# Performance work log

Measured on AMD Instinct MI355X. Metric: run time of the kernel, lower is better.

Reference implementation:

```python
import jax, jax.numpy as jnp
import numpy as np

D_OUT = 256  # out_channels; fourier dim F = D_OUT (Wr has F/2 rows)

def _fourier_pos(H, W, Wr, w1, b1, w2, b2):
    # normalized (H,W) grid in [-1,1], shape [L,2]
    ys = jnp.linspace(-1.0, 1.0, H)
    xs = jnp.linspace(-1.0, 1.0, W)
    gy, gx = jnp.meshgrid(ys, xs, indexing='ij')
    grid = jnp.stack([gy, gx], axis=-1).reshape(-1, 2)  # [L,2]
    proj = grid @ Wr.T                                   # [L,F/2]
    F = 2 * Wr.shape[0]
    feats = jnp.concatenate([jnp.cos(proj), jnp.sin(proj)], axis=-1) / jnp.sqrt(jnp.float32(F))
    h = jax.nn.gelu(feats @ w1.T + b1)
    return h @ w2.T + b2                                 # [L,D_OUT]

def setup_inputs() -> dict:
    key = jax.random.key(0)
    ks = jax.random.split(key, 11)
    N, D, H, W = 16, 256, 128, 128
    s = 1.0 / np.sqrt(D)
    return {
        'x': jax.random.normal(ks[0], (N, D, H, W), jnp.float32),
        'query': jax.random.normal(ks[1], (D_OUT,), jnp.float32),
        'k_w': jax.random.normal(ks[2], (D_OUT, D), jnp.float32) * s,
        'k_b': jax.random.normal(ks[3], (D_OUT,), jnp.float32) * 0.01,
        'v_w': jax.random.normal(ks[4], (D_OUT, D), jnp.float32) * s,
        'v_b': jax.random.normal(ks[5], (D_OUT,), jnp.float32) * 0.01,
        'Wr': jax.random.normal(ks[6], (D_OUT // 2, 2), jnp.float32),
        'w1': jax.random.normal(ks[7], (D_OUT, D_OUT), jnp.float32) * (1.0 / np.sqrt(D_OUT)),
        'b1': jax.random.normal(ks[8], (D_OUT,), jnp.float32) * 0.01,
        'w2': jax.random.normal(ks[9], (D_OUT, D_OUT), jnp.float32) * (1.0 / np.sqrt(D_OUT)),
        'b2': jax.random.normal(ks[10], (D_OUT,), jnp.float32) * 0.01,
    }

def reference(x, query, k_w, k_b, v_w, v_b, Wr, w1, b1, w2, b2):
    N, D, H, W = x.shape
    L = H * W
    tok = x.reshape(N, D, L).transpose(0, 2, 1)          # [N,L,D]
    pos = _fourier_pos(H, W, Wr, w1, b1, w2, b2)         # [L,D_OUT]
    K = tok @ k_w.T + k_b + pos[None]                    # [N,L,D_OUT]
    V = tok @ v_w.T + v_b                                # [N,L,D_OUT]
    scores = jnp.einsum('nld,d->nl', K, query) / jnp.sqrt(jnp.float32(query.shape[0]))
    attn = jax.nn.softmax(scores, axis=1)                # [N,L]
    return jnp.einsum('nl,nld->nd', attn, V)             # [N,D_OUT]
```

## Files before the change

kernel.cpp:

```cpp
#include <hip/hip_runtime.h>
#include <math.h>

#define NB 16
#define DD 256
#define LL 16384
#define DO 256

#define WS_QK    0
#define WS_QW2   256
#define WS_C1    512
#define WS_C2    513
#define WS_W1T   768
#define WS_VWT   (WS_W1T + 65536)
#define WS_PQ    (WS_VWT + 65536)
#define WS_M     (WS_PQ + LL)
#define WS_DEN   (WS_M + NB*32)
#define WS_NUM   (WS_DEN + NB*32)

__device__ __forceinline__ float gelu_tanh(float u) {
    float u3 = u*u*u;
    return 0.5f*u*(1.0f + tanhf(0.7978845608028654f*(u + 0.044715f*u3)));
}

__global__ __launch_bounds__(256) void k0a(const float* __restrict__ query,
        const float* __restrict__ k_w, const float* __restrict__ k_b,
        const float* __restrict__ w2, const float* __restrict__ b2,
        float* __restrict__ ws) {
    __shared__ float q_s[DO];
    __shared__ float red[256];
    int t = threadIdx.x;
    q_s[t] = query[t];
    __syncthreads();
    float aqk = 0.f, aqw = 0.f;
    for (int o = 0; o < DO; ++o) {
        aqk += k_w[o*DD + t] * q_s[o];
        aqw += w2[o*DO + t] * q_s[o];
    }
    ws[WS_QK + t] = aqk;
    ws[WS_QW2 + t] = aqw;
    red[t] = k_b[t]*q_s[t];
    __syncthreads();
    for (int s = 128; s > 0; s >>= 1) { if (t < s) red[t] += red[t+s]; __syncthreads(); }
    if (t == 0) ws[WS_C1] = red[0];
    __syncthreads();
    red[t] = b2[t]*q_s[t];
    __syncthreads();
    for (int s = 128; s > 0; s >>= 1) { if (t < s) red[t] += red[t+s]; __syncthreads(); }
    if (t == 0) ws[WS_C2] = red[0];
}

__global__ __launch_bounds__(256) void k0b(const float* __restrict__ w1,
        const float* __restrict__ v_w, float* __restrict__ ws) {
    int t = threadIdx.x, b = blockIdx.x;
    if (b < 256) {
        ws[WS_W1T + b*DO + t] = w1[t*DO + b];
    } else {
        int c = b - 256;
        ws[WS_VWT + c*DO + t] = v_w[t*DD + c];
    }
}

__global__ __launch_bounds__(256) void k1_pq(const float* __restrict__ Wr,
        const float* __restrict__ b1, float* __restrict__ ws) {
    __shared__ float feats[32*256];
    __shared__ float wbuf[32*256];
    int t = threadIdx.x;
    int w = t >> 6, lane = t & 63;
    int l0 = blockIdx.x * 32;
    int r = t & 127;
    float wr0 = Wr[r*2], wr1 = Wr[r*2+1];
    bool is_cos = (t < 128);
    for (int lr = 0; lr < 32; ++lr) {
        int l = l0 + lr;
        int i = l >> 7, j = l & 127;
        float y = -1.0f + (2.0f/127.0f)*(float)i;
        float xg = -1.0f + (2.0f/127.0f)*(float)j;
        float p = y*wr0 + xg*wr1;
        feats[lr*256 + t] = (is_cos ? cosf(p) : sinf(p)) * 0.0625f;
    }
    int o4 = lane * 4;
    float z[8][4];
    #pragma unroll
    for (int a = 0; a < 8; ++a) { z[a][0]=0.f; z[a][1]=0.f; z[a][2]=0.f; z[a][3]=0.f; }
    __syncthreads();
    for (int fc = 0; fc < 8; ++fc) {
        #pragma unroll
        for (int i2 = 0; i2 < 8; ++i2) {
            int idx = i2*256 + t;
            int fl = idx >> 6;
            int c = (idx & 63) * 4;
            *(float4*)(wbuf + fl*256 + c) =
                *(const float4*)(ws + WS_W1T + (fc*32+fl)*DO + c);
        }
        __syncthreads();
        for (int f = 0; f < 32; ++f) {
            float4 wv = *(const float4*)(wbuf + f*256 + o4);
            #pragma unroll
            for (int lr = 0; lr < 8; ++lr) {
                float fv = feats[(w*8+lr)*256 + fc*32 + f];
                z[lr][0] += fv*wv.x; z[lr][1] += fv*wv.y;
                z[lr][2] += fv*wv.z; z[lr][3] += fv*wv.w;
            }
        }
        __syncthreads();
    }
    float4 b1v = *(const float4*)(b1 + o4);
    float4 qwv = *(const float4*)(ws + WS_QW2 + o4);
    float c2 = ws[WS_C2];
    #pragma unroll
    for (int lr = 0; lr < 8; ++lr) {
        float pp = gelu_tanh(z[lr][0]+b1v.x)*qwv.x + gelu_tanh(z[lr][1]+b1v.y)*qwv.y
                 + gelu_tanh(z[lr][2]+b1v.z)*qwv.z + gelu_tanh(z[lr][3]+b1v.w)*qwv.w;
        for (int off = 32; off > 0; off >>= 1) pp += __shfl_xor(pp, off);
        if (lane == 0) ws[WS_PQ + l0 + w*8 + lr] = pp + c2;
    }
}

__global__ __launch_bounds__(256) void k2_main(const float* __restrict__ x,
        float* __restrict__ ws) {
    __shared__ float tile[DD*65];
    __shared__ float qk_s[DD];
    __shared__ float e_s[64];
    __shared__ float part[256];
    __shared__ float m_s, den_s, sc_s;
    int t = threadIdx.x;
    int n = blockIdx.x >> 5, lb = blockIdx.x & 31;
    const float* xb = x + (size_t)n * DD * LL;
    qk_s[t] = ws[WS_QK + t];
    if (t == 0) { m_s = -INFINITY; den_s = 0.f; sc_s = 0.f; }
    float c1 = ws[WS_C1];
    float num = 0.f;
    int w = t >> 6, lane = t & 63;
    int dld = t >> 4;
    int li = (t & 15) * 4;
    for (int tb = 0; tb < 8; ++tb) {
        int l0 = lb*512 + tb*64;
        __syncthreads();
        #pragma unroll 4
        for (int i2 = 0; i2 < 16; ++i2) {
            int d = i2*16 + dld;
            float4 v = *(const float4*)(xb + (size_t)d*LL + l0 + li);
            float* dst = tile + d*65 + li;
            dst[0]=v.x; dst[1]=v.y; dst[2]=v.z; dst[3]=v.w;
        }
        __syncthreads();
        float acc = 0.f;
        int dbase = w*64;
        #pragma unroll 8
        for (int i2 = 0; i2 < 64; ++i2)
            acc += tile[(dbase+i2)*65 + lane] * qk_s[dbase+i2];
        part[t] = acc;
        __syncthreads();
        if (t < 64) {
            float dot = part[t] + part[64+t] + part[128+t] + part[192+t];
            float score = (dot + c1 + ws[WS_PQ + l0 + t]) * 0.0625f;
            float mc = score;
            for (int off=32; off>0; off>>=1) mc = fmaxf(mc, __shfl_xor(mc, off));
            float mold = m_s;
            float mnew = fmaxf(mold, mc);
            float e = expf(score - mnew);
            e_s[t] = e;
            float dc = e;
            for (int off=32; off>0; off>>=1) dc += __shfl_xor(dc, off);
            if (t == 0) {
                float sc = expf(mold - mnew);
                den_s = den_s*sc + dc;
                m_s = mnew;
                sc_s = sc;
            }
        }
        __syncthreads();
        float sc = sc_s;
        float acc2 = 0.f;
        #pragma unroll 8
        for (int l = 0; l < 64; ++l)
            acc2 += e_s[l] * tile[t*65 + l];
        num = num*sc + acc2;
    }
    int pb = n*32 + lb;
    ws[WS_NUM + pb*256 + t] = num;
    if (t == 0) { ws[WS_M + pb] = m_s; ws[WS_DEN + pb] = den_s; }
}

__global__ __launch_bounds__(256) void k3_final(const float* __restrict__ ws,
        const float* __restrict__ v_b, float* __restrict__ out) {
    __shared__ float s_s[DD];
    int t = threadIdx.x, n = blockIdx.x;
    float m = -INFINITY;
    for (int lb = 0; lb < 32; ++lb) m = fmaxf(m, ws[WS_M + n*32 + lb]);
    float den = 0.f;
    for (int lb = 0; lb < 32; ++lb)
        den += ws[WS_DEN + n*32 + lb] * expf(ws[WS_M + n*32 + lb] - m);
    float sacc = 0.f;
    for (int lb = 0; lb < 32; ++lb) {
        float sc = expf(ws[WS_M + n*32 + lb] - m);
        sacc += ws[WS_NUM + (n*32+lb)*256 + t] * sc;
    }
    s_s[t] = sacc / den;
    __syncthreads();
    float acc = v_b[t];
    for (int d = 0; d < DD; ++d)
        acc += ws[WS_VWT + d*DO + t] * s_s[d];
    out[n*DO + t] = acc;
}

extern "C" void kernel_launch(void* const* d_in, const int* in_sizes, int n_in,
                              void* d_out, int out_size, void* d_ws, size_t ws_size,
                              hipStream_t stream) {
    const float* x     = (const float*)d_in[0];
    const float* query = (const float*)d_in[1];
    const float* k_w   = (const float*)d_in[2];
    const float* k_b   = (const float*)d_in[3];
    const float* v_w   = (const float*)d_in[4];
    const float* v_b   = (const float*)d_in[5];
    const float* Wr    = (const float*)d_in[6];
    const float* w1    = (const float*)d_in[7];
    const float* b1    = (const float*)d_in[8];
    const float* w2    = (const float*)d_in[9];
    const float* b2    = (const float*)d_in[10];
    float* ws  = (float*)d_ws;
    float* out = (float*)d_out;

    k0a<<<1, 256, 0, stream>>>(query, k_w, k_b, w2, b2, ws);
    k0b<<<512, 256, 0, stream>>>(w1, v_w, ws);
    k1_pq<<<512, 256, 0, stream>>>(Wr, b1, ws);
    k2_main<<<512, 256, 0, stream>>>(x, ws);
    k3_final<<<16, 256, 0, stream>>>(ws, v_b, out);
}
```

Baseline: 478.9 us.

## Keep x tiles in registers in main kernel and split sequence into more chunks

The main attention kernel no longer stages each 256x64 x tile in a padded shared-memory buffer. Each thread now keeps its 16 float4 loads in registers and reuses them for both the score dot product and the weighted value accumulation, with small shared-memory reductions for partial scores and the final per-channel sums. The sequence is split into 64 chunks instead of 32, doubling the block count, and launch bounds request higher occupancy. The prologue kernel is spread over 4 blocks and the fourier MLP inner loop is unrolled by two, at the cost of more register pressure and a larger final combine.

New measurement: 564.2 us. 17.8% more time.

```diff
diff --git a/kernel.cpp b/kernel.cpp
--- a/kernel.cpp
+++ b/kernel.cpp
@@ -5,6 +5,10 @@
 #define DD 256
 #define LL 16384
 #define DO 256
+#define NCH 64
+#define CHL 256
+#define NT 4
+#define TL 64
 
 #define WS_QK    0
 #define WS_QW2   256
@@ -14,8 +18,8 @@
 #define WS_VWT   (WS_W1T + 65536)
 #define WS_PQ    (WS_VWT + 65536)
 #define WS_M     (WS_PQ + LL)
-#define WS_DEN   (WS_M + NB*32)
-#define WS_NUM   (WS_DEN + NB*32)
+#define WS_DEN   (WS_M + NB*NCH)
+#define WS_NUM   (WS_DEN + NB*NCH)
 
 __device__ __forceinline__ float gelu_tanh(float u) {
     float u3 = u*u*u;
@@ -28,25 +32,30 @@
         float* __restrict__ ws) {
     __shared__ float q_s[DO];
     __shared__ float red[256];
-    int t = threadIdx.x;
+    int t = threadIdx.x, b = blockIdx.x;
     q_s[t] = query[t];
     __syncthreads();
-    float aqk = 0.f, aqw = 0.f;
-    for (int o = 0; o < DO; ++o) {
-        aqk += k_w[o*DD + t] * q_s[o];
-        aqw += w2[o*DO + t] * q_s[o];
-    }
-    ws[WS_QK + t] = aqk;
-    ws[WS_QW2 + t] = aqw;
-    red[t] = k_b[t]*q_s[t];
-    __syncthreads();
-    for (int s = 128; s > 0; s >>= 1) { if (t < s) red[t] += red[t+s]; __syncthreads(); }
-    if (t == 0) ws[WS_C1] = red[0];
-    __syncthreads();
-    red[t] = b2[t]*q_s[t];
-    __syncthreads();
-    for (int s = 128; s > 0; s >>= 1) { if (t < s) red[t] += red[t+s]; __syncthreads(); }
-    if (t == 0) ws[WS_C2] = red[0];
+    if (b == 0) {
+        float a = 0.f;
+        #pragma unroll 8
+        for (int o = 0; o < DO; ++o) a += k_w[o*DD + t] * q_s[o];
+        ws[WS_QK + t] = a;
+    } else if (b == 1) {
+        float a = 0.f;
+        #pragma unroll 8
+        for (int o = 0; o < DO; ++o) a += w2[o*DO + t] * q_s[o];
+        ws[WS_QW2 + t] = a;
+    } else if (b == 2) {
+        red[t] = k_b[t]*q_s[t];
+        __syncthreads();
+        for (int s = 128; s > 0; s >>= 1) { if (t < s) red[t] += red[t+s]; __syncthreads(); }
+        if (t == 0) ws[WS_C1] = red[0];
+    } else {
+        red[t] = b2[t]*q_s[t];
+        __syncthreads();
+        for (int s = 128; s > 0; s >>= 1) { if (t < s) red[t] += red[t+s]; __syncthreads(); }
+        if (t == 0) ws[WS_C2] = red[0];
+    }
 }
 
 __global__ __launch_bounds__(256) void k0b(const float* __restrict__ w1,
@@ -93,13 +102,16 @@
                 *(const float4*)(ws + WS_W1T + (fc*32+fl)*DO + c);
         }
         __syncthreads();
-        for (int f = 0; f < 32; ++f) {
-            float4 wv = *(const float4*)(wbuf + f*256 + o4);
+        for (int f = 0; f < 32; f += 2) {
+            float4 wv0 = *(const float4*)(wbuf + f*256 + o4);
+            float4 wv1 = *(const float4*)(wbuf + (f+1)*256 + o4);
             #pragma unroll
             for (int lr = 0; lr < 8; ++lr) {
-                float fv = feats[(w*8+lr)*256 + fc*32 + f];
-                z[lr][0] += fv*wv.x; z[lr][1] += fv*wv.y;
-                z[lr][2] += fv*wv.z; z[lr][3] += fv*wv.w;
+                float2 fv = *(const float2*)(feats + (w*8+lr)*256 + fc*32 + f);
+                z[lr][0] += fv.x*wv0.x + fv.y*wv1.x;
+                z[lr][1] += fv.x*wv0.y + fv.y*wv1.y;
+                z[lr][2] += fv.x*wv0.z + fv.y*wv1.z;
+                z[lr][3] += fv.x*wv0.w + fv.y*wv1.w;
             }
         }
         __syncthreads();
@@ -116,52 +128,59 @@
     }
 }
 
-__global__ __launch_bounds__(256) void k2_main(const float* __restrict__ x,
+__global__ __launch_bounds__(256,4) void k2_main(const float* __restrict__ x,
         float* __restrict__ ws) {
-    __shared__ float tile[DD*65];
-    __shared__ float qk_s[DD];
+    __shared__ float part2[16*68];
     __shared__ float e_s[64];
-    __shared__ float part[256];
+    __shared__ float numred[256*17];
     __shared__ float m_s, den_s, sc_s;
     int t = threadIdx.x;
-    int n = blockIdx.x >> 5, lb = blockIdx.x & 31;
-    const float* xb = x + (size_t)n * DD * LL;
-    qk_s[t] = ws[WS_QK + t];
+    int n = blockIdx.x >> 6, ch = blockIdx.x & 63;
+    const float* xb = x + (size_t)n * (size_t)(DD*LL);
+    int dld = t >> 4;
+    int li  = (t & 15) * 4;
+    float qkr[16];
+    #pragma unroll
+    for (int i2 = 0; i2 < 16; ++i2) qkr[i2] = ws[WS_QK + i2*16 + dld];
+    float c1 = ws[WS_C1];
     if (t == 0) { m_s = -INFINITY; den_s = 0.f; sc_s = 0.f; }
-    float c1 = ws[WS_C1];
-    float num = 0.f;
-    int w = t >> 6, lane = t & 63;
-    int dld = t >> 4;
-    int li = (t & 15) * 4;
-    for (int tb = 0; tb < 8; ++tb) {
-        int l0 = lb*512 + tb*64;
-        __syncthreads();
-        #pragma unroll 4
+    float num[16];
+    #pragma unroll
+    for (int i2 = 0; i2 < 16; ++i2) num[i2] = 0.f;
+
+    for (int tb = 0; tb < NT; ++tb) {
+        int l0 = ch*CHL + tb*TL;
+        float4 xr[16];
+        #pragma unroll
         for (int i2 = 0; i2 < 16; ++i2) {
             int d = i2*16 + dld;
-            float4 v = *(const float4*)(xb + (size_t)d*LL + l0 + li);
-            float* dst = tile + d*65 + li;
-            dst[0]=v.x; dst[1]=v.y; dst[2]=v.z; dst[3]=v.w;
-        }
-        __syncthreads();
-        float acc = 0.f;
-        int dbase = w*64;
-        #pragma unroll 8
-        for (int i2 = 0; i2 < 64; ++i2)
-            acc += tile[(dbase+i2)*65 + lane] * qk_s[dbase+i2];
-        part[t] = acc;
+            xr[i2] = *(const float4*)(xb + (size_t)d*LL + l0 + li);
+        }
+        float4 sp = make_float4(0.f, 0.f, 0.f, 0.f);
+        #pragma unroll
+        for (int i2 = 0; i2 < 16; ++i2) {
+            sp.x += xr[i2].x * qkr[i2];
+            sp.y += xr[i2].y * qkr[i2];
+            sp.z += xr[i2].z * qkr[i2];
+            sp.w += xr[i2].w * qkr[i2];
+        }
+        *(float4*)(part2 + dld*68 + li) = sp;
         __syncthreads();
         if (t < 64) {
-            float dot = part[t] + part[64+t] + part[128+t] + part[192+t];
+            float dot = 0.f;
+            #pragma unroll
+            for (int j = 0; j < 16; ++j) dot += part2[j*68 + t];
             float score = (dot + c1 + ws[WS_PQ + l0 + t]) * 0.0625f;
             float mc = score;
-            for (int off=32; off>0; off>>=1) mc = fmaxf(mc, __shfl_xor(mc, off));
+            #pragma unroll
+            for (int off = 32; off > 0; off >>= 1) mc = fmaxf(mc, __shfl_xor(mc, off));
             float mold = m_s;
             float mnew = fmaxf(mold, mc);
             float e = expf(score - mnew);
             e_s[t] = e;
             float dc = e;
-            for (int off=32; off>0; off>>=1) dc += __shfl_xor(dc, off);
+            #pragma unroll
+            for (int off = 32; off > 0; off >>= 1) dc += __shfl_xor(dc, off);
             if (t == 0) {
                 float sc = expf(mold - mnew);
                 den_s = den_s*sc + dc;
@@ -170,15 +189,24 @@
             }
         }
         __syncthreads();
+        float4 ef = *(const float4*)(e_s + li);
         float sc = sc_s;
-        float acc2 = 0.f;
-        #pragma unroll 8
-        for (int l = 0; l < 64; ++l)
-            acc2 += e_s[l] * tile[t*65 + l];
-        num = num*sc + acc2;
-    }
-    int pb = n*32 + lb;
-    ws[WS_NUM + pb*256 + t] = num;
+        #pragma unroll
+        for (int i2 = 0; i2 < 16; ++i2)
+            num[i2] = num[i2]*sc
+                    + xr[i2].x*ef.x + xr[i2].y*ef.y + xr[i2].z*ef.z + xr[i2].w*ef.w;
+        __syncthreads();
+    }
+    int g = t & 15;
+    #pragma unroll
+    for (int i2 = 0; i2 < 16; ++i2)
+        numred[(i2*16 + dld)*17 + g] = num[i2];
+    __syncthreads();
+    float acc = 0.f;
+    #pragma unroll
+    for (int gg = 0; gg < 16; ++gg) acc += numred[t*17 + gg];
+    int pb = n*NCH + ch;
+    ws[WS_NUM + (size_t)pb*256 + t] = acc;
     if (t == 0) { ws[WS_M + pb] = m_s; ws[WS_DEN + pb] = den_s; }
 }
 
@@ -187,18 +215,19 @@
     __shared__ float s_s[DD];
     int t = threadIdx.x, n = blockIdx.x;
     float m = -INFINITY;
-    for (int lb = 0; lb < 32; ++lb) m = fmaxf(m, ws[WS_M + n*32 + lb]);
+    for (int ch = 0; ch < NCH; ++ch) m = fmaxf(m, ws[WS_M + n*NCH + ch]);
     float den = 0.f;
-    for (int lb = 0; lb < 32; ++lb)
-        den += ws[WS_DEN + n*32 + lb] * expf(ws[WS_M + n*32 + lb] - m);
+    for (int ch = 0; ch < NCH; ++ch)
+        den += ws[WS_DEN + n*NCH + ch] * expf(ws[WS_M + n*NCH + ch] - m);
     float sacc = 0.f;
-    for (int lb = 0; lb < 32; ++lb) {
-        float sc = expf(ws[WS_M + n*32 + lb] - m);
-        sacc += ws[WS_NUM + (n*32+lb)*256 + t] * sc;
+    for (int ch = 0; ch < NCH; ++ch) {
+        float sc = expf(ws[WS_M + n*NCH + ch] - m);
+        sacc += ws[WS_NUM + (size_t)(n*NCH+ch)*256 + t] * sc;
     }
     s_s[t] = sacc / den;
     __syncthreads();
     float acc = v_b[t];
+    #pragma unroll 8
     for (int d = 0; d < DD; ++d)
         acc += ws[WS_VWT + d*DO + t] * s_s[d];
     out[n*DO + t] = acc;
@@ -221,9 +250,9 @@
     float* ws  = (float*)d_ws;
     float* out = (float*)d_out;
 
-    k0a<<<1, 256, 0, stream>>>(query, k_w, k_b, w2, b2, ws);
+    k0a<<<4, 256, 0, stream>>>(query, k_w, k_b, w2, b2, ws);
     k0b<<<512, 256, 0, stream>>>(w1, v_w, ws);
     k1_pq<<<512, 256, 0, stream>>>(Wr, b1, ws);
-    k2_main<<<512, 256, 0, stream>>>(x, ws);
+    k2_main<<<1024, 256, 0, stream>>>(x, ws);
     k3_final<<<16, 256, 0, stream>>>(ws, v_b, out);
 }
```
